# Kernel optimization log

Measured on AMD Instinct MI355X. Metric: run time of the kernel, lower is better.

## Reference

```python
import jax, jax.numpy as jnp
import numpy as np

# Fingertip landmark indices (end_ldmrk = [12,24,36,48,57] in flat coords -> landmarks {4,8,12,16,19})
_END_LANDMARKS = {4, 8, 12, 16, 19}

def _build_pairs():
    pairs = []
    for j in range(20):  # index in range(0, 60, 3) -> landmark j = index//3
        start = j + 1 if j in _END_LANDMARKS else j + 2  # skip adjacent landmark unless fingertip
        for k in range(start, 21):  # x in range(start, 63, 3) -> landmark k = x//3
            pairs.append((j, k))
    return np.asarray(pairs, dtype=np.int32)  # [195, 2]

_PAIRS = _build_pairs()
_I = jnp.asarray(_PAIRS[:, 0])  # [195]
_J = jnp.asarray(_PAIRS[:, 1])  # [195]


def setup_inputs() -> dict:
    key = jax.random.key(0)
    B = 1_000_000
    return {"tensor": jax.random.normal(key, (B, 63), dtype=jnp.float32)}


def reference(tensor):
    # tensor: [B, 63] = 21 landmarks x (x, y, z); distances use only x, y.
    B = tensor.shape[0]
    xy = tensor.reshape(B, 21, 3)[..., :2]          # [B, 21, 2]
    d = xy[:, _I, :] - xy[:, _J, :]                 # [B, 195, 2] only needed pairs
    feats = jnp.sqrt(jnp.sum(d * d, axis=-1))       # [B, 195] 2D Euclidean distances
    return jnp.concatenate([tensor, feats], axis=-1)  # [B, 258]
```

## Files before the change

kernel.cpp:

```cpp
#include <hip/hip_runtime.h>
#include <math.h>

#define ROWS_PER_BLOCK 16
#define NPAIRS 195
#define NTHREADS 256
#define ROW_OUT 258
#define NLM 21

typedef float f32x4 __attribute__((ext_vector_type(4)));

struct CodeTab { unsigned int c[NPAIRS]; };

constexpr CodeTab make_codes() {
    CodeTab t{};
    int n = 0;
    for (int a = 0; a < 20; ++a) {
        bool tip = (a == 4) || (a == 8) || (a == 12) || (a == 16) || (a == 19);
        int start = tip ? a + 1 : a + 2;
        for (int b = start; b < 21; ++b) {
            t.c[n] = (unsigned int)a | ((unsigned int)b << 16);
            ++n;
        }
    }
    return t;
}

__constant__ CodeTab CODES = make_codes();

__global__ __launch_bounds__(NTHREADS)
void HandKineticLayer_18545668784560_kernel(const float* __restrict__ in,
                                            float* __restrict__ out,
                                            int B) {
    __shared__ __align__(16) float tile[ROWS_PER_BLOCK * ROW_OUT];
    __shared__ float2 xy2[ROWS_PER_BLOCK * NLM];

    const int rowBase = blockIdx.x * ROWS_PER_BLOCK;
    const int t = threadIdx.x;
    const int nrows = min(ROWS_PER_BLOCK, B - rowBase);
    if (nrows <= 0) return;

    if (nrows == ROWS_PER_BLOCK) {
        const f32x4* __restrict__ in4 =
            reinterpret_cast<const f32x4*>(in + (size_t)rowBase * 63);
        if (t < 252) {
            const f32x4 v = __builtin_nontemporal_load(&in4[t]);
            const int f = t * 4;
#pragma unroll
            for (int e = 0; e < 4; ++e) {
                const int g = f + e;
                const int row = g / 63;
                const int col = g - row * 63;
                tile[row * ROW_OUT + col] = v[e];
                const int lm = col / 3;
                const int c3 = col - lm * 3;
                if (c3 == 0) xy2[row * NLM + lm].x = v[e];
                else if (c3 == 1) xy2[row * NLM + lm].y = v[e];
            }
        }
    } else {
        const int nelem = nrows * 63;
        for (int g = t; g < nelem; g += NTHREADS) {
            const float val = in[(size_t)rowBase * 63 + g];
            const int row = g / 63;
            const int col = g - row * 63;
            tile[row * ROW_OUT + col] = val;
            const int lm = col / 3;
            const int c3 = col - lm * 3;
            if (c3 == 0) xy2[row * NLM + lm].x = val;
            else if (c3 == 1) xy2[row * NLM + lm].y = val;
        }
    }

    __syncthreads();

    if (nrows == ROWS_PER_BLOCK) {
#pragma unroll
        for (int k = 0; k < 13; ++k) {
            const int idx = t + k * NTHREADS;
            if (idx < ROWS_PER_BLOCK * NPAIRS) {
                const int row = idx / NPAIRS;
                const int p = idx - row * NPAIRS;
                const unsigned int c = CODES.c[p];
                const float2 a = xy2[row * NLM + (int)(c & 0xffu)];
                const float2 b = xy2[row * NLM + (int)(c >> 16)];
                const float dx = a.x - b.x;
                const float dy = a.y - b.y;
                tile[row * ROW_OUT + 63 + p] = sqrtf(dx * dx + dy * dy);
            }
        }
    } else {
        const int total = nrows * NPAIRS;
        for (int idx = t; idx < total; idx += NTHREADS) {
            const int row = idx / NPAIRS;
            const int p = idx - row * NPAIRS;
            const unsigned int c = CODES.c[p];
            const float2 a = xy2[row * NLM + (int)(c & 0xffu)];
            const float2 b = xy2[row * NLM + (int)(c >> 16)];
            const float dx = a.x - b.x;
            const float dy = a.y - b.y;
            tile[row * ROW_OUT + 63 + p] = sqrtf(dx * dx + dy * dy);
        }
    }

    __syncthreads();

    if (nrows == ROWS_PER_BLOCK) {
        const f32x4* __restrict__ tl4 = reinterpret_cast<const f32x4*>(tile);
        f32x4* __restrict__ o4 =
            reinterpret_cast<f32x4*>(out + (size_t)rowBase * ROW_OUT);
#pragma unroll
        for (int k = t; k < (ROWS_PER_BLOCK * ROW_OUT) / 4; k += NTHREADS) {
            __builtin_nontemporal_store(tl4[k], &o4[k]);
        }
    } else {
        const int nout = nrows * ROW_OUT;
        for (int k = t; k < nout; k += NTHREADS) {
            out[(size_t)rowBase * ROW_OUT + k] = tile[k];
        }
    }
}

extern "C" void kernel_launch(void* const* d_in, const int* in_sizes, int n_in,
                              void* d_out, int out_size, void* d_ws, size_t ws_size,
                              hipStream_t stream) {
    const float* in = (const float*)d_in[0];
    float* out = (float*)d_out;
    const int B = in_sizes[0] / 63;
    const int blocks = (B + ROWS_PER_BLOCK - 1) / ROWS_PER_BLOCK;
    hipLaunchKernelGGL(HandKineticLayer_18545668784560_kernel,
                       dim3(blocks), dim3(NTHREADS), 0, stream,
                       in, out, B);
}
```

Baseline: 283.7 us.

## Use persistent grid with double-buffered tiles and register prefetch of next tile

```diff
diff --git a/kernel.cpp b/kernel.cpp
--- a/kernel.cpp
+++ b/kernel.cpp
@@ -1,11 +1,13 @@
 #include <hip/hip_runtime.h>
 #include <math.h>
 
-#define ROWS_PER_BLOCK 16
+#define ROWS 16
 #define NPAIRS 195
 #define NTHREADS 256
 #define ROW_OUT 258
 #define NLM 21
+#define TILE_F (ROWS * ROW_OUT)
+#define GRID 1024
 
 typedef float f32x4 __attribute__((ext_vector_type(4)));
 
@@ -27,70 +29,30 @@
 
 __constant__ CodeTab CODES = make_codes();
 
-__global__ __launch_bounds__(NTHREADS)
-void HandKineticLayer_18545668784560_kernel(const float* __restrict__ in,
-                                            float* __restrict__ out,
-                                            int B) {
-    __shared__ __align__(16) float tile[ROWS_PER_BLOCK * ROW_OUT];
-    __shared__ float2 xy2[ROWS_PER_BLOCK * NLM];
+__device__ __forceinline__ void scatter_tile(float* __restrict__ tile,
+                                             float2* __restrict__ xy2,
+                                             const f32x4 v, int t) {
+    const int f = t * 4;
+#pragma unroll
+    for (int e = 0; e < 4; ++e) {
+        const int g = f + e;
+        const int row = g / 63;
+        const int col = g - row * 63;
+        tile[row * ROW_OUT + col] = v[e];
+        const int lm = col / 3;
+        const int c3 = col - lm * 3;
+        if (c3 == 0) xy2[row * NLM + lm].x = v[e];
+        else if (c3 == 1) xy2[row * NLM + lm].y = v[e];
+    }
+}
 
-    const int rowBase = blockIdx.x * ROWS_PER_BLOCK;
-    const int t = threadIdx.x;
-    const int nrows = min(ROWS_PER_BLOCK, B - rowBase);
-    if (nrows <= 0) return;
-
-    if (nrows == ROWS_PER_BLOCK) {
-        const f32x4* __restrict__ in4 =
-            reinterpret_cast<const f32x4*>(in + (size_t)rowBase * 63);
-        if (t < 252) {
-            const f32x4 v = __builtin_nontemporal_load(&in4[t]);
-            const int f = t * 4;
+__device__ __forceinline__ void compute_dists(float* __restrict__ tile,
+                                              const float2* __restrict__ xy2,
+                                              int t) {
 #pragma unroll
-            for (int e = 0; e < 4; ++e) {
-                const int g = f + e;
-                const int row = g / 63;
-                const int col = g - row * 63;
-                tile[row * ROW_OUT + col] = v[e];
-                const int lm = col / 3;
-                const int c3 = col - lm * 3;
-                if (c3 == 0) xy2[row * NLM + lm].x = v[e];
-                else if (c3 == 1) xy2[row * NLM + lm].y = v[e];
-            }
-        }
-    } else {
-        const int nelem = nrows * 63;
-        for (int g = t; g < nelem; g += NTHREADS) {
-            const float val = in[(size_t)rowBase * 63 + g];
-            const int row = g / 63;
-            const int col = g - row * 63;
-            tile[row * ROW_OUT + col] = val;
-            const int lm = col / 3;
-            const int c3 = col - lm * 3;
-            if (c3 == 0) xy2[row * NLM + lm].x = val;
-            else if (c3 == 1) xy2[row * NLM + lm].y = val;
-        }
-    }
-
-    __syncthreads();
-
-    if (nrows == ROWS_PER_BLOCK) {
-#pragma unroll
-        for (int k = 0; k < 13; ++k) {
-            const int idx = t + k * NTHREADS;
-            if (idx < ROWS_PER_BLOCK * NPAIRS) {
-                const int row = idx / NPAIRS;
-                const int p = idx - row * NPAIRS;
-                const unsigned int c = CODES.c[p];
-                const float2 a = xy2[row * NLM + (int)(c & 0xffu)];
-                const float2 b = xy2[row * NLM + (int)(c >> 16)];
-                const float dx = a.x - b.x;
-                const float dy = a.y - b.y;
-                tile[row * ROW_OUT + 63 + p] = sqrtf(dx * dx + dy * dy);
-            }
-        }
-    } else {
-        const int total = nrows * NPAIRS;
-        for (int idx = t; idx < total; idx += NTHREADS) {
+    for (int k = 0; k < 13; ++k) {
+        const int idx = t + k * NTHREADS;
+        if (idx < ROWS * NPAIRS) {
             const int row = idx / NPAIRS;
             const int p = idx - row * NPAIRS;
             const unsigned int c = CODES.c[p];
@@ -101,21 +63,91 @@
             tile[row * ROW_OUT + 63 + p] = sqrtf(dx * dx + dy * dy);
         }
     }
+}
 
-    __syncthreads();
+__global__ __launch_bounds__(NTHREADS)
+void HandKineticLayer_18545668784560_kernel(const float* __restrict__ in,
+                                            float* __restrict__ out,
+                                            int B) {
+    __shared__ __align__(16) float tile[2][TILE_F];
+    __shared__ float2 xy2[2][ROWS * NLM];
 
-    if (nrows == ROWS_PER_BLOCK) {
-        const f32x4* __restrict__ tl4 = reinterpret_cast<const f32x4*>(tile);
-        f32x4* __restrict__ o4 =
-            reinterpret_cast<f32x4*>(out + (size_t)rowBase * ROW_OUT);
+    const int t = threadIdx.x;
+    const int ntiles = B / ROWS;
+
+    const int tile0 = blockIdx.x;
+    if (tile0 < ntiles) {
+        if (t < 252) {
+            const f32x4* __restrict__ in4 =
+                reinterpret_cast<const f32x4*>(in + (size_t)tile0 * (ROWS * 63));
+            const f32x4 v = __builtin_nontemporal_load(&in4[t]);
+            scatter_tile(tile[0], xy2[0], v, t);
+        }
+        __syncthreads();
+    }
+
+    int i = 0;
+    for (int tl = tile0; tl < ntiles; tl += GRID, ++i) {
+        const int cur = i & 1;
+        const int nxt = tl + GRID;
+        f32x4 vn{};
+        const bool have_next = (nxt < ntiles) && (t < 252);
+        if (have_next) {
+            const f32x4* __restrict__ in4 =
+                reinterpret_cast<const f32x4*>(in + (size_t)nxt * (ROWS * 63));
+            vn = __builtin_nontemporal_load(&in4[t]);
+        }
+
+        compute_dists(tile[cur], xy2[cur], t);
+        __syncthreads();
+
+        {
+            const f32x4* __restrict__ tl4 =
+                reinterpret_cast<const f32x4*>(&tile[cur][0]);
+            f32x4* __restrict__ o4 =
+                reinterpret_cast<f32x4*>(out + (size_t)tl * TILE_F);
 #pragma unroll
-        for (int k = t; k < (ROWS_PER_BLOCK * ROW_OUT) / 4; k += NTHREADS) {
-            __builtin_nontemporal_store(tl4[k], &o4[k]);
+            for (int k = t; k < TILE_F / 4; k += NTHREADS) {
+                __builtin_nontemporal_store(tl4[k], &o4[k]);
+            }
         }
-    } else {
-        const int nout = nrows * ROW_OUT;
+
+        if (have_next) {
+            scatter_tile(tile[cur ^ 1], xy2[cur ^ 1], vn, t);
+        }
+        __syncthreads();
+    }
+
+    const int rem = B - ntiles * ROWS;
+    if (rem > 0 && blockIdx.x == (unsigned)(ntiles % GRID)) {
+        const int rowBase = ntiles * ROWS;
+        const int nelem = rem * 63;
+        for (int g = t; g < nelem; g += NTHREADS) {
+            const float val = in[(size_t)rowBase * 63 + g];
+            const int row = g / 63;
+            const int col = g - row * 63;
+            tile[0][row * ROW_OUT + col] = val;
+            const int lm = col / 3;
+            const int c3 = col - lm * 3;
+            if (c3 == 0) xy2[0][row * NLM + lm].x = val;
+            else if (c3 == 1) xy2[0][row * NLM + lm].y = val;
+        }
+        __syncthreads();
+        const int total = rem * NPAIRS;
+        for (int idx = t; idx < total; idx += NTHREADS) {
+            const int row = idx / NPAIRS;
+            const int p = idx - row * NPAIRS;
+            const unsigned int c = CODES.c[p];
+            const float2 a = xy2[0][row * NLM + (int)(c & 0xffu)];
+            const float2 b = xy2[0][row * NLM + (int)(c >> 16)];
+            const float dx = a.x - b.x;
+            const float dy = a.y - b.y;
+            tile[0][row * ROW_OUT + 63 + p] = sqrtf(dx * dx + dy * dy);
+        }
+        __syncthreads();
+        const int nout = rem * ROW_OUT;
         for (int k = t; k < nout; k += NTHREADS) {
-            out[(size_t)rowBase * ROW_OUT + k] = tile[k];
+            out[(size_t)rowBase * ROW_OUT + k] = tile[0][k];
         }
     }
 }
@@ -126,8 +158,7 @@
     const float* in = (const float*)d_in[0];
     float* out = (float*)d_out;
     const int B = in_sizes[0] / 63;
-    const int blocks = (B + ROWS_PER_BLOCK - 1) / ROWS_PER_BLOCK;
     hipLaunchKernelGGL(HandKineticLayer_18545668784560_kernel,
-                       dim3(blocks), dim3(NTHREADS), 0, stream,
+                       dim3(GRID), dim3(NTHREADS), 0, stream,
                        in, out, B);
 }
```

New measurement: 272.2 us. 1.04x faster.
